# Kernel tuning notes

Hardware: AMD Instinct MI355X
Metric: run time of the kernel (lower is better)

## Reference

```python
import jax, jax.numpy as jnp
import numpy as np

N_NODES = 100000
N_EDGES = 1000000
D_IN = 64
FEATURES = [64, 64, 16]


def setup_inputs() -> dict:
    key = jax.random.key(0)
    ks = jax.random.split(key, 10)
    nodes = jax.random.normal(ks[0], (N_NODES, D_IN), dtype=jnp.float32)
    senders = jax.random.randint(ks[1], (N_EDGES,), 0, N_NODES, dtype=jnp.int64)
    receivers = jax.random.randint(ks[2], (N_EDGES,), 0, N_NODES, dtype=jnp.int64)
    dims = [D_IN] + FEATURES
    params = {}
    for i in range(len(FEATURES)):
        fan_in = dims[i]
        # hk.Linear default: truncated-normal-ish init; plain normal scaled is fine for a reference
        params[f"W{i}"] = jax.random.normal(ks[3 + i], (dims[i], dims[i + 1]), dtype=jnp.float32) / np.sqrt(fan_in)
        params[f"b{i}"] = jnp.zeros((dims[i + 1],), dtype=jnp.float32)
    return {"nodes": nodes, "senders": senders, "receivers": receivers, **params}


def _gcn_layer(h, senders, receivers, W, b, use_tanh, add_self_edges):
    N = h.shape[0]
    h = h @ W + b
    if use_tanh:
        h = jnp.tanh(h)
    if add_self_edges:
        self_idx = jnp.arange(N, dtype=senders.dtype)
        s = jnp.concatenate([senders, self_idx], axis=0)
        r = jnp.concatenate([receivers, self_idx], axis=0)
    else:
        s, r = senders, receivers
    ones = jnp.ones(s.shape, dtype=h.dtype)
    deg_s = jax.ops.segment_sum(ones, s, num_segments=N)
    deg_r = jax.ops.segment_sum(ones, r, num_segments=N)
    h = h * jax.lax.rsqrt(jnp.maximum(deg_s, 1.0))[:, None]
    h = jax.ops.segment_sum(h[s], r, num_segments=N)  # gather -> scatter-add
    h = h * jax.lax.rsqrt(jnp.maximum(deg_r, 1.0))[:, None]
    return h


def reference(nodes, senders, receivers, W0, b0, W1, b1, W2, b2):
    h = nodes
    # layers over features[:-1]: tanh activation, self edges added
    h = _gcn_layer(h, senders, receivers, W0, b0, use_tanh=True, add_self_edges=True)
    h = _gcn_layer(h, senders, receivers, W1, b1, use_tanh=True, add_self_edges=True)
    # final layer: linear only, no self edges, still symmetric normalization
    h = _gcn_layer(h, senders, receivers, W2, b2, use_tanh=False, add_self_edges=False)
    return h
```

## Files before the change

kernel.cpp:

```cpp
#include <hip/hip_runtime.h>


#define CAP 32
#define BSH 7
#define BW 128
#define BCAP 1664
#define EPT 16

typedef unsigned short u16;
typedef unsigned int u32;

__device__ __forceinline__ float bf2f(u16 u) {
    return __uint_as_float(((u32)u) << 16);
}
__device__ __forceinline__ u16 f2bf(float f) {
    u32 x = __float_as_uint(f);
    u32 r = x + 0x7fff + ((x >> 16) & 1);
    return (u16)(r >> 16);
}
__device__ __forceinline__ float fast_tanh(float x) {
    x = fminf(15.f, fmaxf(-15.f, x));
    float e = __expf(2.f * x);
    return (e - 1.f) / (e + 1.f);
}
__device__ __forceinline__ int unpack_deg(const u32* pk, int n) {
    return (int)((pk[n >> 2] >> (8 * (n & 3))) & 255u);
}

__global__ __launch_bounds__(256) void k_init(int* __restrict__ curR,
                                              int* __restrict__ curS, int nbuk) {
    int t = blockIdx.x * 256 + threadIdx.x;
    if (t < nbuk) {
        curR[t] = t * BCAP;
        curS[t] = t * BCAP;
    }
}

__global__ __launch_bounds__(1024) void k_part(const int* __restrict__ s,
                                               const int* __restrict__ r,
                                               int* __restrict__ curR,
                                               int* __restrict__ curS,
                                               int2* __restrict__ pairR,
                                               int* __restrict__ svalS,
                                               int E, int nbuk) {
    __shared__ int cR[1024], cS[1024], bR[1024], bS[1024];
    const int t = threadIdx.x;
    for (int i = t; i < nbuk; i += 1024) { cR[i] = 0; cS[i] = 0; }
    __syncthreads();

    int ss[EPT], rr[EPT];
    const int base = blockIdx.x * (1024 * EPT);
#pragma unroll
    for (int i = 0; i < EPT; ++i) {
        int e = base + i * 1024 + t;
        ss[i] = (e < E) ? s[e] : -1;
        rr[i] = (e < E) ? r[e] : -1;
    }
#pragma unroll
    for (int i = 0; i < EPT; ++i) {
        if (rr[i] >= 0) {
            atomicAdd(&cR[rr[i] >> BSH], 1);
            atomicAdd(&cS[ss[i] >> BSH], 1);
        }
    }
    __syncthreads();
    for (int i = t; i < nbuk; i += 1024) {
        bR[i] = cR[i] ? atomicAdd(&curR[i], cR[i]) : 0;
        bS[i] = cS[i] ? atomicAdd(&curS[i], cS[i]) : 0;
    }
    __syncthreads();
    for (int i = t; i < nbuk; i += 1024) { cR[i] = 0; cS[i] = 0; }
    __syncthreads();
#pragma unroll
    for (int i = 0; i < EPT; ++i) {
        if (rr[i] >= 0) {
            int rb = rr[i] >> BSH;
            int pos = bR[rb] + atomicAdd(&cR[rb], 1);
            if (pos < (rb + 1) * BCAP) pairR[pos] = make_int2(ss[i], rr[i]);
            int sb = ss[i] >> BSH;
            int ps = bS[sb] + atomicAdd(&cS[sb], 1);
            if (ps < (sb + 1) * BCAP) svalS[ps] = ss[i];
        }
    }
}

__global__ __launch_bounds__(256) void k_ellb(const int2* __restrict__ pairR,
                                              const int* __restrict__ curR,
                                              int* __restrict__ ell,
                                              u32* __restrict__ degIp) {
    __shared__ int degLoc[BW];
    const int b = blockIdx.x, t = threadIdx.x;
    if (t < BW) degLoc[t] = 0;
    __syncthreads();
    const int start = b * BCAP;
    const int cnt = min(curR[b] - start, BCAP);
    for (int e = t; e < cnt; e += 256) {
        int2 p = pairR[start + e];
        int slot = atomicAdd(&degLoc[p.y - (b << BSH)], 1);
        if (slot < CAP) ell[p.y * CAP + slot] = p.x;
    }
    __syncthreads();
    if (t < BW / 4) {
        u32 w = (u32)min(degLoc[4 * t], 255) |
                ((u32)min(degLoc[4 * t + 1], 255) << 8) |
                ((u32)min(degLoc[4 * t + 2], 255) << 16) |
                ((u32)min(degLoc[4 * t + 3], 255) << 24);
        degIp[(b << (BSH - 2)) + t] = w;
    }
}

__global__ __launch_bounds__(256) void k_dego(const int* __restrict__ svalS,
                                              const int* __restrict__ curS,
                                              u32* __restrict__ degOp) {
    __shared__ int degLoc[BW];
    const int b = blockIdx.x, t = threadIdx.x;
    if (t < BW) degLoc[t] = 0;
    __syncthreads();
    const int start = b * BCAP;
    const int cnt = min(curS[b] - start, BCAP);
    for (int e = t; e < cnt; e += 256) {
        atomicAdd(&degLoc[svalS[start + e] - (b << BSH)], 1);
    }
    __syncthreads();
    if (t < BW / 4) {
        u32 w = (u32)min(degLoc[4 * t], 255) |
                ((u32)min(degLoc[4 * t + 1], 255) << 8) |
                ((u32)min(degLoc[4 * t + 2], 255) << 16) |
                ((u32)min(degLoc[4 * t + 3], 255) << 24);
        degOp[(b << (BSH - 2)) + t] = w;
    }
}

__global__ __launch_bounds__(256) void k_transform64(const float* __restrict__ in,
                                                     const float* __restrict__ W,
                                                     const float* __restrict__ b,
                                                     const u32* __restrict__ degOp,
                                                     u16* __restrict__ out, int N) {
    __shared__ float4 lds[4][128];
    const int lane = threadIdx.x & 63;
    const int wv = threadIdx.x >> 6;

    float wc[64];
#pragma unroll
    for (int k = 0; k < 64; ++k) wc[k] = W[k * 64 + lane];
    const float bias = b[lane];

    const int base = blockIdx.x * 32 + wv * 8;
    const float4* in4 = (const float4*)in;
#pragma unroll
    for (int r2 = 0; r2 < 2; ++r2) {
        int idx = r2 * 64 + lane;
        int nn = base + (idx >> 4);
        float4 v = {0.f, 0.f, 0.f, 0.f};
        if (nn < N) v = in4[(size_t)base * 16 + idx];
        lds[wv][idx] = v;
    }
#pragma unroll
    for (int i = 0; i < 8; ++i) {
        const int n = base + i;
        if (n >= N) break;
        float acc = 0.f;
#pragma unroll
        for (int kk = 0; kk < 16; ++kk) {
            float4 h = lds[wv][i * 16 + kk];
            acc = fmaf(h.x, wc[4 * kk + 0], acc);
            acc = fmaf(h.y, wc[4 * kk + 1], acc);
            acc = fmaf(h.z, wc[4 * kk + 2], acc);
            acc = fmaf(h.w, wc[4 * kk + 3], acc);
        }
        float as01 = rsqrtf((float)unpack_deg(degOp, n) + 1.f);
        acc = fast_tanh(acc + bias) * as01;
        out[(size_t)n * 64 + lane] = f2bf(acc);
    }
}

__global__ __launch_bounds__(256) void k_fgt64(const u16* __restrict__ h,
                                               const u32* __restrict__ degOp,
                                               const u32* __restrict__ degIp,
                                               const int* __restrict__ ell,
                                               const float* __restrict__ W,
                                               const float* __restrict__ b,
                                               u16* __restrict__ y, int N) {
    __shared__ float4 lds[4][16];
    const int lane = threadIdx.x & 63;
    const int wv = threadIdx.x >> 6;
    const int g = lane >> 4, c = lane & 15;

    float wc[64];
#pragma unroll
    for (int k = 0; k < 64; ++k) wc[k] = W[k * 64 + lane];
    const float bias = b[lane];

    const ushort4* h4 = (const ushort4*)h;
    const int base = blockIdx.x * 32 + wv * 8;
    for (int i8 = 0; i8 < 8; ++i8) {
        const int n = base + i8;
        if (n >= N) break;
        const int di = unpack_deg(degIp, n);
        const int deg = min(di, CAP);
        int idxv = (lane < CAP) ? ell[n * CAP + lane] : 0;

        float4 acc = {0.f, 0.f, 0.f, 0.f};
        const int jn = (deg + 3) >> 2;
        for (int j = 0; j < jn; ++j) {
            int i = g + 4 * j;
            int id = __shfl(idxv, i, 64);
            if (i < deg) {
                ushort4 v = h4[(size_t)id * 16 + c];
                acc.x += bf2f(v.x); acc.y += bf2f(v.y);
                acc.z += bf2f(v.z); acc.w += bf2f(v.w);
            }
        }
#pragma unroll
        for (int m = 16; m <= 32; m <<= 1) {
            acc.x += __shfl_xor(acc.x, m, 64);
            acc.y += __shfl_xor(acc.y, m, 64);
            acc.z += __shfl_xor(acc.z, m, 64);
            acc.w += __shfl_xor(acc.w, m, 64);
        }
        ushort4 sv = h4[(size_t)n * 16 + c];
        acc.x += bf2f(sv.x); acc.y += bf2f(sv.y);
        acc.z += bf2f(sv.z); acc.w += bf2f(sv.w);
        if (g == 0) lds[wv][c] = acc;

        const float inscale = rsqrtf((float)di + 1.f);
        const float outscale = rsqrtf((float)unpack_deg(degOp, n) + 1.f);
        float dot = 0.f;
        const float* row = (const float*)lds[wv];
#pragma unroll
        for (int k = 0; k < 64; k += 4) {
            float4 hh = *(const float4*)(row + k);
            dot = fmaf(hh.x, wc[k + 0], dot);
            dot = fmaf(hh.y, wc[k + 1], dot);
            dot = fmaf(hh.z, wc[k + 2], dot);
            dot = fmaf(hh.w, wc[k + 3], dot);
        }
        float v = fast_tanh(fmaf(dot, inscale, bias)) * outscale;
        y[(size_t)n * 64 + lane] = f2bf(v);
    }
}

__global__ __launch_bounds__(256) void k_fgt16(const u16* __restrict__ h,
                                               const u32* __restrict__ degOp,
                                               const u32* __restrict__ degIp,
                                               const int* __restrict__ ell,
                                               const float* __restrict__ W,
                                               const float* __restrict__ b,
                                               u16* __restrict__ y16, int N) {
    __shared__ float4 lds[4][16];
    const int lane = threadIdx.x & 63;
    const int wv = threadIdx.x >> 6;
    const int g = lane >> 4, c = lane & 15;
    const int j = lane & 15;

    float wc[16];
#pragma unroll
    for (int kk = 0; kk < 16; ++kk) wc[kk] = W[(16 * g + kk) * 16 + j];
    const float bias = b[j];

    const ushort4* h4 = (const ushort4*)h;
    const int base = blockIdx.x * 32 + wv * 8;
    for (int i8 = 0; i8 < 8; ++i8) {
        const int n = base + i8;
        if (n >= N) break;
        const int di = unpack_deg(degIp, n);
        const int deg = min(di, CAP);
        int idxv = (lane < CAP) ? ell[n * CAP + lane] : 0;

        float4 acc = {0.f, 0.f, 0.f, 0.f};
        const int jn = (deg + 3) >> 2;
        for (int jj = 0; jj < jn; ++jj) {
            int i = g + 4 * jj;
            int id = __shfl(idxv, i, 64);
            if (i < deg) {
                ushort4 v = h4[(size_t)id * 16 + c];
                acc.x += bf2f(v.x); acc.y += bf2f(v.y);
                acc.z += bf2f(v.z); acc.w += bf2f(v.w);
            }
        }
#pragma unroll
        for (int m = 16; m <= 32; m <<= 1) {
            acc.x += __shfl_xor(acc.x, m, 64);
            acc.y += __shfl_xor(acc.y, m, 64);
            acc.z += __shfl_xor(acc.z, m, 64);
            acc.w += __shfl_xor(acc.w, m, 64);
        }
        ushort4 sv = h4[(size_t)n * 16 + c];
        acc.x += bf2f(sv.x); acc.y += bf2f(sv.y);
        acc.z += bf2f(sv.z); acc.w += bf2f(sv.w);
        if (g == 0) lds[wv][c] = acc;

        const float* row = (const float*)lds[wv];
        float dot = 0.f;
#pragma unroll
        for (int kk = 0; kk < 16; ++kk) dot = fmaf(row[16 * g + kk], wc[kk], dot);
#pragma unroll
        for (int m = 16; m <= 32; m <<= 1) dot += __shfl_xor(dot, m, 64);

        if (g == 0) {
            const float inscale = rsqrtf((float)di + 1.f);
            const float outscale = rsqrtf(fmaxf((float)unpack_deg(degOp, n), 1.f));
            float v = fmaf(dot, inscale, bias) * outscale;
            y16[(size_t)n * 16 + j] = f2bf(v);
        }
    }
}

__global__ __launch_bounds__(256) void k_g16(const u16* __restrict__ h,
                                             const u32* __restrict__ degIp,
                                             const int* __restrict__ ell,
                                             float* __restrict__ out, int N) {
    const int lane = threadIdx.x & 63;
    const int wv = threadIdx.x >> 6;
    const int n = blockIdx.x * 4 + wv;
    if (n >= N) return;
    const int g = lane >> 2, c = lane & 3;
    const int di = unpack_deg(degIp, n);
    const int deg = min(di, CAP);
    int idxv = (lane < CAP) ? ell[n * CAP + lane] : 0;

    const ushort4* h4 = (const ushort4*)h;
    float4 acc = {0.f, 0.f, 0.f, 0.f};
    const int jn = (deg + 15) >> 4;
    for (int j = 0; j < jn; ++j) {
        int i = g + 16 * j;
        int id = __shfl(idxv, i, 64);
        if (i < deg) {
            ushort4 v = h4[(size_t)id * 4 + c];
            acc.x += bf2f(v.x); acc.y += bf2f(v.y);
            acc.z += bf2f(v.z); acc.w += bf2f(v.w);
        }
    }
#pragma unroll
    for (int m = 4; m <= 32; m <<= 1) {
        acc.x += __shfl_xor(acc.x, m, 64);
        acc.y += __shfl_xor(acc.y, m, 64);
        acc.z += __shfl_xor(acc.z, m, 64);
        acc.w += __shfl_xor(acc.w, m, 64);
    }
    if (g == 0) {
        float sc = rsqrtf(fmaxf((float)di, 1.f));
        acc.x *= sc; acc.y *= sc; acc.z *= sc; acc.w *= sc;
        ((float4*)out)[(size_t)n * 4 + c] = acc;
    }
}

extern "C" void kernel_launch(void* const* d_in, const int* in_sizes, int n_in,
                              void* d_out, int out_size, void* d_ws, size_t ws_size,
                              hipStream_t stream) {
    const float* nodes = (const float*)d_in[0];
    const int* senders = (const int*)d_in[1];
    const int* receivers = (const int*)d_in[2];
    const float* W0 = (const float*)d_in[3];
    const float* b0 = (const float*)d_in[4];
    const float* W1 = (const float*)d_in[5];
    const float* b1 = (const float*)d_in[6];
    const float* W2 = (const float*)d_in[7];
    const float* b2 = (const float*)d_in[8];
    float* out = (float*)d_out;

    const int N = in_sizes[0] / 64;
    const int E = in_sizes[1];
    const int nbuk = (N + BW - 1) >> BSH;
    const int nwords = nbuk * (BW / 4);

    u16* A = (u16*)d_ws;
    u16* B = A + (size_t)N * 64;
    u16* Y16 = B + (size_t)N * 64;
    u32* degOp = (u32*)(Y16 + (size_t)N * 16);
    u32* degIp = degOp + nwords;
    int* curR = (int*)(degIp + nwords);
    int* curS = curR + nbuk;
    int* ell = (int*)(curS + nbuk);
    int2* pairR = (int2*)(ell + (size_t)N * CAP);
    int* svalS = (int*)(pairR + (size_t)nbuk * BCAP);

    k_init<<<(nbuk + 255) / 256, 256, 0, stream>>>(curR, curS, nbuk);
    const int pblk = (E + 1024 * EPT - 1) / (1024 * EPT);
    k_part<<<pblk, 1024, 0, stream>>>(senders, receivers, curR, curS,
                                      pairR, svalS, E, nbuk);
    k_ellb<<<nbuk, 256, 0, stream>>>(pairR, curR, ell, degIp);
    k_dego<<<nbuk, 256, 0, stream>>>(svalS, curS, degOp);

    const int tb = (N + 31) / 32;
    const int fb = (N + 31) / 32;
    const int gb = (N + 3) / 4;

    k_transform64<<<tb, 256, 0, stream>>>(nodes, W0, b0, degOp, A, N);
    k_fgt64<<<fb, 256, 0, stream>>>(A, degOp, degIp, ell, W1, b1, B, N);
    k_fgt16<<<fb, 256, 0, stream>>>(B, degOp, degIp, ell, W2, b2, Y16, N);
    k_g16<<<gb, 256, 0, stream>>>(Y16, degIp, ell, out, N);
}
```

Before: 272.4 us.

## Compact partition records, merge degree kernels, prefetch ELL rows and software-pipeline gathers

Partition records shrink to a packed u32 (sender plus local receiver) and u8 sender-local bytes, and bucket counters become relative offsets zeroed by a memset, which removes the init kernel. The in-degree/ELL build and out-degree kernels are merged into one launch. EPT drops from 16 to 4 so the partition kernel runs more blocks. The fused gather kernels prefetch the next node's ELL row and double-buffer the neighbour loads, and the final gather processes 8 nodes per wave. These aim to cut preprocessing traffic and launch count and to hide gather latency, at the cost of more registers and a 20-bit limit on node indices.

```diff
diff --git a/kernel.cpp b/kernel.cpp
--- a/kernel.cpp
+++ b/kernel.cpp
@@ -5,8 +5,9 @@
 #define BSH 7
 #define BW 128
 #define BCAP 1664
-#define EPT 16
-
+#define EPT 4
+
+typedef unsigned char u8;
 typedef unsigned short u16;
 typedef unsigned int u32;
 
@@ -27,21 +28,12 @@
     return (int)((pk[n >> 2] >> (8 * (n & 3))) & 255u);
 }
 
-__global__ __launch_bounds__(256) void k_init(int* __restrict__ curR,
-                                              int* __restrict__ curS, int nbuk) {
-    int t = blockIdx.x * 256 + threadIdx.x;
-    if (t < nbuk) {
-        curR[t] = t * BCAP;
-        curS[t] = t * BCAP;
-    }
-}
-
 __global__ __launch_bounds__(1024) void k_part(const int* __restrict__ s,
                                                const int* __restrict__ r,
                                                int* __restrict__ curR,
                                                int* __restrict__ curS,
-                                               int2* __restrict__ pairR,
-                                               int* __restrict__ svalS,
+                                               u32* __restrict__ pairR,
+                                               u8* __restrict__ svalS,
                                                int E, int nbuk) {
     __shared__ int cR[1024], cS[1024], bR[1024], bS[1024];
     const int t = threadIdx.x;
@@ -75,59 +67,59 @@
     for (int i = 0; i < EPT; ++i) {
         if (rr[i] >= 0) {
             int rb = rr[i] >> BSH;
+            int rloc = rr[i] & (BW - 1);
             int pos = bR[rb] + atomicAdd(&cR[rb], 1);
-            if (pos < (rb + 1) * BCAP) pairR[pos] = make_int2(ss[i], rr[i]);
+            if (pos < BCAP) pairR[rb * BCAP + pos] = (u32)ss[i] | ((u32)rloc << 20);
             int sb = ss[i] >> BSH;
             int ps = bS[sb] + atomicAdd(&cS[sb], 1);
-            if (ps < (sb + 1) * BCAP) svalS[ps] = ss[i];
-        }
-    }
-}
-
-__global__ __launch_bounds__(256) void k_ellb(const int2* __restrict__ pairR,
+            if (ps < BCAP) svalS[sb * BCAP + ps] = (u8)(ss[i] & (BW - 1));
+        }
+    }
+}
+
+__global__ __launch_bounds__(256) void k_bdeg(const u32* __restrict__ pairR,
+                                              const u8* __restrict__ svalS,
                                               const int* __restrict__ curR,
+                                              const int* __restrict__ curS,
                                               int* __restrict__ ell,
-                                              u32* __restrict__ degIp) {
+                                              u32* __restrict__ degIp,
+                                              u32* __restrict__ degOp, int nbuk) {
     __shared__ int degLoc[BW];
-    const int b = blockIdx.x, t = threadIdx.x;
+    const int t = threadIdx.x;
     if (t < BW) degLoc[t] = 0;
     __syncthreads();
-    const int start = b * BCAP;
-    const int cnt = min(curR[b] - start, BCAP);
-    for (int e = t; e < cnt; e += 256) {
-        int2 p = pairR[start + e];
-        int slot = atomicAdd(&degLoc[p.y - (b << BSH)], 1);
-        if (slot < CAP) ell[p.y * CAP + slot] = p.x;
-    }
-    __syncthreads();
-    if (t < BW / 4) {
-        u32 w = (u32)min(degLoc[4 * t], 255) |
-                ((u32)min(degLoc[4 * t + 1], 255) << 8) |
-                ((u32)min(degLoc[4 * t + 2], 255) << 16) |
-                ((u32)min(degLoc[4 * t + 3], 255) << 24);
-        degIp[(b << (BSH - 2)) + t] = w;
-    }
-}
-
-__global__ __launch_bounds__(256) void k_dego(const int* __restrict__ svalS,
-                                              const int* __restrict__ curS,
-                                              u32* __restrict__ degOp) {
-    __shared__ int degLoc[BW];
-    const int b = blockIdx.x, t = threadIdx.x;
-    if (t < BW) degLoc[t] = 0;
-    __syncthreads();
-    const int start = b * BCAP;
-    const int cnt = min(curS[b] - start, BCAP);
-    for (int e = t; e < cnt; e += 256) {
-        atomicAdd(&degLoc[svalS[start + e] - (b << BSH)], 1);
-    }
-    __syncthreads();
-    if (t < BW / 4) {
-        u32 w = (u32)min(degLoc[4 * t], 255) |
-                ((u32)min(degLoc[4 * t + 1], 255) << 8) |
-                ((u32)min(degLoc[4 * t + 2], 255) << 16) |
-                ((u32)min(degLoc[4 * t + 3], 255) << 24);
-        degOp[(b << (BSH - 2)) + t] = w;
+    if (blockIdx.x < (unsigned)nbuk) {
+        const int b = blockIdx.x;
+        const int cnt = min(curR[b], BCAP);
+        for (int e = t; e < cnt; e += 256) {
+            u32 p = pairR[b * BCAP + e];
+            int sidx = (int)(p & 0xFFFFFu);
+            int rloc = (int)(p >> 20);
+            int slot = atomicAdd(&degLoc[rloc], 1);
+            if (slot < CAP) ell[((b << BSH) + rloc) * CAP + slot] = sidx;
+        }
+        __syncthreads();
+        if (t < BW / 4) {
+            u32 w = (u32)min(degLoc[4 * t], 255) |
+                    ((u32)min(degLoc[4 * t + 1], 255) << 8) |
+                    ((u32)min(degLoc[4 * t + 2], 255) << 16) |
+                    ((u32)min(degLoc[4 * t + 3], 255) << 24);
+            degIp[(b << (BSH - 2)) + t] = w;
+        }
+    } else {
+        const int b = blockIdx.x - nbuk;
+        const int cnt = min(curS[b], BCAP);
+        for (int e = t; e < cnt; e += 256) {
+            atomicAdd(&degLoc[(int)svalS[b * BCAP + e]], 1);
+        }
+        __syncthreads();
+        if (t < BW / 4) {
+            u32 w = (u32)min(degLoc[4 * t], 255) |
+                    ((u32)min(degLoc[4 * t + 1], 255) << 8) |
+                    ((u32)min(degLoc[4 * t + 2], 255) << 16) |
+                    ((u32)min(degLoc[4 * t + 3], 255) << 24);
+            degOp[(b << (BSH - 2)) + t] = w;
+        }
     }
 }
 
@@ -193,24 +185,36 @@
 
     const ushort4* h4 = (const ushort4*)h;
     const int base = blockIdx.x * 32 + wv * 8;
+    int idxv = 0;
+    if (lane < CAP && base < N) idxv = ell[base * CAP + lane];
     for (int i8 = 0; i8 < 8; ++i8) {
         const int n = base + i8;
         if (n >= N) break;
         const int di = unpack_deg(degIp, n);
         const int deg = min(di, CAP);
-        int idxv = (lane < CAP) ? ell[n * CAP + lane] : 0;
+        const int jn = (deg + 3) >> 2;
 
         float4 acc = {0.f, 0.f, 0.f, 0.f};
-        const int jn = (deg + 3) >> 2;
-        for (int j = 0; j < jn; ++j) {
+        ushort4 v = {0, 0, 0, 0};
+        {
+            int id0 = __shfl(idxv, g, 64);
+            if (g < deg) v = h4[(size_t)id0 * 16 + c];
+        }
+        for (int j = 1; j < jn; ++j) {
             int i = g + 4 * j;
-            int id = __shfl(idxv, i, 64);
-            if (i < deg) {
-                ushort4 v = h4[(size_t)id * 16 + c];
-                acc.x += bf2f(v.x); acc.y += bf2f(v.y);
-                acc.z += bf2f(v.z); acc.w += bf2f(v.w);
-            }
-        }
+            int idn = __shfl(idxv, i & 31, 64);
+            ushort4 vn = {0, 0, 0, 0};
+            if (i < deg) vn = h4[(size_t)idn * 16 + c];
+            acc.x += bf2f(v.x); acc.y += bf2f(v.y);
+            acc.z += bf2f(v.z); acc.w += bf2f(v.w);
+            v = vn;
+        }
+        acc.x += bf2f(v.x); acc.y += bf2f(v.y);
+        acc.z += bf2f(v.z); acc.w += bf2f(v.w);
+
+        int idxv_n = 0;
+        if (lane < CAP && i8 < 7 && (n + 1) < N) idxv_n = ell[(n + 1) * CAP + lane];
+
 #pragma unroll
         for (int m = 16; m <= 32; m <<= 1) {
             acc.x += __shfl_xor(acc.x, m, 64);
@@ -235,8 +239,9 @@
             dot = fmaf(hh.z, wc[k + 2], dot);
             dot = fmaf(hh.w, wc[k + 3], dot);
         }
-        float v = fast_tanh(fmaf(dot, inscale, bias)) * outscale;
-        y[(size_t)n * 64 + lane] = f2bf(v);
+        float vout = fast_tanh(fmaf(dot, inscale, bias)) * outscale;
+        y[(size_t)n * 64 + lane] = f2bf(vout);
+        idxv = idxv_n;
     }
 }
 
@@ -260,24 +265,36 @@
 
     const ushort4* h4 = (const ushort4*)h;
     const int base = blockIdx.x * 32 + wv * 8;
+    int idxv = 0;
+    if (lane < CAP && base < N) idxv = ell[base * CAP + lane];
     for (int i8 = 0; i8 < 8; ++i8) {
         const int n = base + i8;
         if (n >= N) break;
         const int di = unpack_deg(degIp, n);
         const int deg = min(di, CAP);
-        int idxv = (lane < CAP) ? ell[n * CAP + lane] : 0;
+        const int jn = (deg + 3) >> 2;
 
         float4 acc = {0.f, 0.f, 0.f, 0.f};
-        const int jn = (deg + 3) >> 2;
-        for (int jj = 0; jj < jn; ++jj) {
+        ushort4 v = {0, 0, 0, 0};
+        {
+            int id0 = __shfl(idxv, g, 64);
+            if (g < deg) v = h4[(size_t)id0 * 16 + c];
+        }
+        for (int jj = 1; jj < jn; ++jj) {
             int i = g + 4 * jj;
-            int id = __shfl(idxv, i, 64);
-            if (i < deg) {
-                ushort4 v = h4[(size_t)id * 16 + c];
-                acc.x += bf2f(v.x); acc.y += bf2f(v.y);
-                acc.z += bf2f(v.z); acc.w += bf2f(v.w);
-            }
-        }
+            int idn = __shfl(idxv, i & 31, 64);
+            ushort4 vn = {0, 0, 0, 0};
+            if (i < deg) vn = h4[(size_t)idn * 16 + c];
+            acc.x += bf2f(v.x); acc.y += bf2f(v.y);
+            acc.z += bf2f(v.z); acc.w += bf2f(v.w);
+            v = vn;
+        }
+        acc.x += bf2f(v.x); acc.y += bf2f(v.y);
+        acc.z += bf2f(v.z); acc.w += bf2f(v.w);
+
+        int idxv_n = 0;
+        if (lane < CAP && i8 < 7 && (n + 1) < N) idxv_n = ell[(n + 1) * CAP + lane];
+
 #pragma unroll
         for (int m = 16; m <= 32; m <<= 1) {
             acc.x += __shfl_xor(acc.x, m, 64);
@@ -300,9 +317,10 @@
         if (g == 0) {
             const float inscale = rsqrtf((float)di + 1.f);
             const float outscale = rsqrtf(fmaxf((float)unpack_deg(degOp, n), 1.f));
-            float v = fmaf(dot, inscale, bias) * outscale;
-            y16[(size_t)n * 16 + j] = f2bf(v);
-        }
+            float vout = fmaf(dot, inscale, bias) * outscale;
+            y16[(size_t)n * 16 + j] = f2bf(vout);
+        }
+        idxv = idxv_n;
     }
 }
 
@@ -312,36 +330,43 @@
                                              float* __restrict__ out, int N) {
     const int lane = threadIdx.x & 63;
     const int wv = threadIdx.x >> 6;
-    const int n = blockIdx.x * 4 + wv;
-    if (n >= N) return;
     const int g = lane >> 2, c = lane & 3;
-    const int di = unpack_deg(degIp, n);
-    const int deg = min(di, CAP);
-    int idxv = (lane < CAP) ? ell[n * CAP + lane] : 0;
-
     const ushort4* h4 = (const ushort4*)h;
-    float4 acc = {0.f, 0.f, 0.f, 0.f};
-    const int jn = (deg + 15) >> 4;
-    for (int j = 0; j < jn; ++j) {
-        int i = g + 16 * j;
-        int id = __shfl(idxv, i, 64);
-        if (i < deg) {
-            ushort4 v = h4[(size_t)id * 4 + c];
-            acc.x += bf2f(v.x); acc.y += bf2f(v.y);
-            acc.z += bf2f(v.z); acc.w += bf2f(v.w);
-        }
-    }
-#pragma unroll
-    for (int m = 4; m <= 32; m <<= 1) {
-        acc.x += __shfl_xor(acc.x, m, 64);
-        acc.y += __shfl_xor(acc.y, m, 64);
-        acc.z += __shfl_xor(acc.z, m, 64);
-        acc.w += __shfl_xor(acc.w, m, 64);
-    }
-    if (g == 0) {
-        float sc = rsqrtf(fmaxf((float)di, 1.f));
-        acc.x *= sc; acc.y *= sc; acc.z *= sc; acc.w *= sc;
-        ((float4*)out)[(size_t)n * 4 + c] = acc;
+    const int base = blockIdx.x * 32 + wv * 8;
+    int idxv = 0;
+    if (lane < CAP && base < N) idxv = ell[base * CAP + lane];
+    for (int i8 = 0; i8 < 8; ++i8) {
+        const int n = base + i8;
+        if (n >= N) break;
+        const int di = unpack_deg(degIp, n);
+        const int deg = min(di, CAP);
+
+        float4 acc = {0.f, 0.f, 0.f, 0.f};
+#pragma unroll
+        for (int jj = 0; jj < 2; ++jj) {
+            int i = g + 16 * jj;
+            int id = __shfl(idxv, i, 64);
+            if (i < deg) {
+                ushort4 v = h4[(size_t)id * 4 + c];
+                acc.x += bf2f(v.x); acc.y += bf2f(v.y);
+                acc.z += bf2f(v.z); acc.w += bf2f(v.w);
+            }
+        }
+        int idxv_n = 0;
+        if (lane < CAP && i8 < 7 && (n + 1) < N) idxv_n = ell[(n + 1) * CAP + lane];
+#pragma unroll
+        for (int m = 4; m <= 32; m <<= 1) {
+            acc.x += __shfl_xor(acc.x, m, 64);
+            acc.y += __shfl_xor(acc.y, m, 64);
+            acc.z += __shfl_xor(acc.z, m, 64);
+            acc.w += __shfl_xor(acc.w, m, 64);
+        }
+        if (g == 0) {
+            float sc = rsqrtf(fmaxf((float)di, 1.f));
+            acc.x *= sc; acc.y *= sc; acc.z *= sc; acc.w *= sc;
+            ((float4*)out)[(size_t)n * 4 + c] = acc;
+        }
+        idxv = idxv_n;
     }
 }
 
@@ -372,22 +397,20 @@
     int* curR = (int*)(degIp + nwords);
     int* curS = curR + nbuk;
     int* ell = (int*)(curS + nbuk);
-    int2* pairR = (int2*)(ell + (size_t)N * CAP);
-    int* svalS = (int*)(pairR + (size_t)nbuk * BCAP);
-
-    k_init<<<(nbuk + 255) / 256, 256, 0, stream>>>(curR, curS, nbuk);
+    u32* pairR = (u32*)(ell + (size_t)N * CAP);
+    u8* svalS = (u8*)(pairR + (size_t)nbuk * BCAP);
+
+    hipMemsetAsync(curR, 0, 2 * (size_t)nbuk * sizeof(int), stream);
     const int pblk = (E + 1024 * EPT - 1) / (1024 * EPT);
     k_part<<<pblk, 1024, 0, stream>>>(senders, receivers, curR, curS,
                                       pairR, svalS, E, nbuk);
-    k_ellb<<<nbuk, 256, 0, stream>>>(pairR, curR, ell, degIp);
-    k_dego<<<nbuk, 256, 0, stream>>>(svalS, curS, degOp);
-
-    const int tb = (N + 31) / 32;
+    k_bdeg<<<2 * nbuk, 256, 0, stream>>>(pairR, svalS, curR, curS,
+                                         ell, degIp, degOp, nbuk);
+
     const int fb = (N + 31) / 32;
-    const int gb = (N + 3) / 4;
-
-    k_transform64<<<tb, 256, 0, stream>>>(nodes, W0, b0, degOp, A, N);
+
+    k_transform64<<<fb, 256, 0, stream>>>(nodes, W0, b0, degOp, A, N);
     k_fgt64<<<fb, 256, 0, stream>>>(A, degOp, degIp, ell, W1, b1, B, N);
     k_fgt16<<<fb, 256, 0, stream>>>(B, degOp, degIp, ell, W2, b2, Y16, N);
-    k_g16<<<gb, 256, 0, stream>>>(Y16, degIp, ell, out, N);
-}
+    k_g16<<<fb, 256, 0, stream>>>(Y16, degIp, ell, out, N);
+}
```

Result: no change. 275.7 us (+1.2%).
